# Optimization experiments

Hardware: AMD Instinct MI355X
Metric: run time of the kernel (lower is better)

## Reference

```python
import jax, jax.numpy as jnp
import numpy as np

B, N, D, H, C = 2, 2048, 1024, 16, 3
Dh = D // H


def setup_inputs() -> dict:
    key = jax.random.key(0)
    ks = jax.random.split(key, 6)
    x = jax.random.normal(ks[0], (B, N, D), jnp.float32)
    coords = jax.random.normal(ks[1], (B, N, C), jnp.float32)
    attn_mask = jax.random.normal(ks[2], (N, N), jnp.float32) * 0.1  # additive float bias (2d kind)
    Wqkv = jax.random.normal(ks[3], (D, 3 * D), jnp.float32) / np.sqrt(D)
    bqkv = jax.random.normal(ks[4], (3 * D,), jnp.float32) * 0.01
    rel_weight = jax.random.normal(ks[5], (H, C), jnp.float32) * 0.02
    return {"x": x, "coords": coords, "attn_mask": attn_mask,
            "Wqkv": Wqkv, "bqkv": bqkv, "rel_weight": rel_weight}


def reference(x, coords, attn_mask, Wqkv, bqkv, rel_weight):
    b, n, d = x.shape
    h, dh = rel_weight.shape[0], d // rel_weight.shape[0]
    scale = 1.0 / np.sqrt(float(dh))

    qkv = x @ Wqkv + bqkv                      # [B,N,3D]
    q, k, v = jnp.split(qkv, 3, axis=-1)

    def to_heads(t):
        return t.reshape(b, n, h, dh).transpose(0, 2, 1, 3)  # [B,H,N,Dh]

    qh, kh, vh = to_heads(q), to_heads(k), to_heads(v)

    # scaled dot-product scores (flex_attention applies scale before score_mod)
    scores = jnp.einsum('bhnd,bhmd->bhnm', qh, kh) * scale   # [B,H,N,N]

    # coordinate-derived per-head relative bias: coord_proj[b,h,qi] - coord_proj[b,h,kj]
    coord_proj = jnp.einsum('bnc,hc->bhn', coords.astype(jnp.float32), rel_weight)
    scores = scores + coord_proj[:, :, :, None] - coord_proj[:, :, None, :]

    # additive float mask bias, '2d' kind: shape (N,N) broadcast over B,H
    scores = scores + attn_mask[None, None, :, :]

    attn = jax.nn.softmax(scores, axis=-1)
    out = jnp.einsum('bhnm,bhmd->bhnd', attn, vh)            # [B,H,N,Dh]
    return out.transpose(0, 2, 1, 3).reshape(b, n, d)        # [B,N,D]
```

## Files before the change

### kernel.cpp

```cpp
#include <hip/hip_runtime.h>

typedef _Float16 half8 __attribute__((ext_vector_type(8)));
typedef _Float16 half4 __attribute__((ext_vector_type(4)));
typedef _Float16 half2v __attribute__((ext_vector_type(2)));
typedef float floatx4 __attribute__((ext_vector_type(4)));

#define LOG2E 1.44269504088896f
#define QSCALE 0.18033688011112f

__device__ __forceinline__ void async16(const void* g, void* l) {
    __builtin_amdgcn_global_load_lds(
        (const __attribute__((address_space(1))) unsigned int*)g,
        (__attribute__((address_space(3))) unsigned int*)l, 16, 0, 0);
}
__device__ __forceinline__ half4 pack4(float a, float b, float c, float d) {
    half2v lo = __builtin_bit_cast(half2v, __builtin_amdgcn_cvt_pkrtz(a, b));
    half2v hi = __builtin_bit_cast(half2v, __builtin_amdgcn_cvt_pkrtz(c, d));
    half4 r; r[0] = lo[0]; r[1] = lo[1]; r[2] = hi[0]; r[3] = hi[1];
    return r;
}
__device__ __forceinline__ half8 cat8(half4 lo, half4 hi) {
    half8 r;
    r[0] = lo[0]; r[1] = lo[1]; r[2] = lo[2]; r[3] = lo[3];
    r[4] = hi[0]; r[5] = hi[1]; r[6] = hi[2]; r[7] = hi[3];
    return r;
}

__global__ __launch_bounds__(256) void k_prep(
    const float* __restrict__ x, const float* __restrict__ W,
    const float* __restrict__ coords, const float* __restrict__ rw,
    const float* __restrict__ mask,
    _Float16* __restrict__ xh, _Float16* __restrict__ Wt,
    _Float16* __restrict__ esch, _Float16* __restrict__ maskp) {
    __shared__ float smem[4352];
    int bx = blockIdx.x, tid = threadIdx.x;
    if (bx < 2048) {
        int i = bx * 256 + tid;
        const floatx4* xin = (const floatx4*)x;
        floatx4 a = xin[i * 2];
        floatx4 b = xin[i * 2 + 1];
        half8 h;
        h[0] = (_Float16)a[0]; h[1] = (_Float16)a[1]; h[2] = (_Float16)a[2]; h[3] = (_Float16)a[3];
        h[4] = (_Float16)b[0]; h[5] = (_Float16)b[1]; h[6] = (_Float16)b[2]; h[7] = (_Float16)b[3];
        *(half8*)&xh[i * 8] = h;
    } else if (bx < 5120) {
        int b2 = bx - 2048;
        int n0 = (b2 % 96) * 32, k0 = (b2 / 96) * 32;
        int tx = tid & 31, ty = tid >> 5;
        float (*tile)[33] = (float(*)[33])smem;
        #pragma unroll
        for (int r = 0; r < 4; ++r)
            tile[ty + r * 8][tx] = W[(size_t)(k0 + ty + r * 8) * 3072 + n0 + tx];
        __syncthreads();
        #pragma unroll
        for (int r = 0; r < 4; ++r)
            Wt[(size_t)(n0 + ty + r * 8) * 1024 + k0 + tx] = (_Float16)tile[tx][ty + r * 8];
    } else if (bx < 5376) {
        int idx = (bx - 5120) * 256 + tid;
        int bh = idx >> 11, n = idx & 2047;
        int b = bh >> 4, h = bh & 15;
        const float* c = &coords[(b * 2048 + n) * 3];
        const float* w = &rw[h * 3];
        float v = -LOG2E * (c[0] * w[0] + c[1] * w[1] + c[2] * w[2]);
        esch[idx] = (_Float16)__builtin_amdgcn_exp2f(v);
    } else {
        int bid = bx - 5376;
        int qt = bid >> 5, kt = bid & 31;
        int row0 = qt * 64, col0 = kt * 64;
        int lr = tid >> 2, lc = (tid & 3) * 16;
        #pragma unroll
        for (int j = 0; j < 4; ++j)
            *(floatx4*)&smem[lr * 68 + lc + j * 4] =
                *(const floatx4*)&mask[(size_t)(row0 + lr) * 2048 + col0 + lc + j * 4];
        __syncthreads();
        int w = tid >> 6, lane = tid & 63, quad = lane >> 4, l16 = lane & 15;
        half4* outp = (half4*)maskp + (size_t)((qt * 32 + kt) * 4 + w) * 256 + lane;
        #pragma unroll
        for (int t = 0; t < 4; ++t) {
            floatx4 m = *(const floatx4*)&smem[(w * 16 + l16) * 68 + t * 16 + quad * 4];
            outp[t * 64] = pack4(m[0] * LOG2E, m[1] * LOG2E, m[2] * LOG2E, m[3] * LOG2E);
        }
    }
}

__global__ __launch_bounds__(256) void k_gemm(
    const _Float16* __restrict__ Ah, const _Float16* __restrict__ Bt,
    const float* __restrict__ bias, const _Float16* __restrict__ esch,
    _Float16* __restrict__ qh, _Float16* __restrict__ kh, _Float16* __restrict__ vt) {
    __shared__ _Float16 smem[16384];
    int tid = threadIdx.x;
    int w = tid >> 6, lane = tid & 63;
    int quad = lane >> 4, l16 = lane & 15;
    int m0 = blockIdx.y * 128;
    int n0 = blockIdx.x * 128;
    bool QK = n0 < 2048;
    int mq = (w >> 1) * 64, nq = (w & 1) * 64;
    int c0 = n0 + nq;

    int rl4 = lane >> 2;
    int pb4 = lane & 3;
    floatx4 acc[4][4] = {};

    const _Float16* ap[2];
    const _Float16* bp[2];
    #pragma unroll
    for (int j = 0; j < 2; ++j) {
        int row = w * 32 + j * 16 + rl4;
        int lb = pb4 ^ (row & 3) ^ ((row >> 2) & 3);
        ap[j] = Ah + (size_t)(m0 + row) * 1024 + lb * 8;
        bp[j] = Bt + (size_t)(n0 + row) * 1024 + lb * 8;
    }

    #define GSTAGE(buf) {                                      \
        _Float16* As_ = smem + (buf) * 8192;                   \
        _Float16* Bs_ = As_ + 4096;                            \
        async16(ap[0], &As_[(w * 32) * 32]);                   \
        async16(ap[1], &As_[(w * 32 + 16) * 32]);              \
        async16(bp[0], &Bs_[(w * 32) * 32]);                   \
        async16(bp[1], &Bs_[(w * 32 + 16) * 32]);              \
        ap[0] += 32; ap[1] += 32; bp[0] += 32; bp[1] += 32;    \
    }

    #define GBODY(cur, last) {                                                         \
        __syncthreads();                                                               \
        if (!(last)) GSTAGE((cur) ^ 1);                                                \
        const _Float16* As_ = smem + (cur) * 8192;                                     \
        const _Float16* Bs_ = As_ + 4096;                                              \
        half8 af[4], bf[4];                                                            \
        _Pragma("unroll")                                                              \
        for (int s = 0; s < 4; ++s) {                                                  \
            int ra = mq + s * 16 + l16;                                                \
            af[s] = *(const half8*)&As_[ra * 32 +                                      \
                ((quad ^ (ra & 3) ^ ((ra >> 2) & 3)) << 3)];                           \
            int rb = nq + s * 16 + l16;                                                \
            bf[s] = *(const half8*)&Bs_[rb * 32 +                                      \
                ((quad ^ (rb & 3) ^ ((rb >> 2) & 3)) << 3)];                           \
        }                                                                              \
        if (QK) {                                                                      \
            _Pragma("unroll")                                                          \
            for (int ms = 0; ms < 4; ++ms)                                             \
                _Pragma("unroll")                                                      \
                for (int ns = 0; ns < 4; ++ns)                                         \
                    acc[ms][ns] = __builtin_amdgcn_mfma_f32_16x16x32_f16(              \
                        bf[ns], af[ms], acc[ms][ns], 0, 0, 0);                         \
        } else {                                                                       \
            _Pragma("unroll")                                                          \
            for (int ms = 0; ms < 4; ++ms)                                             \
                _Pragma("unroll")                                                      \
                for (int ns = 0; ns < 4; ++ns)                                         \
                    acc[ms][ns] = __builtin_amdgcn_mfma_f32_16x16x32_f16(              \
                        af[ms], bf[ns], acc[ms][ns], 0, 0, 0);                         \
        }                                                                              \
    }

    GSTAGE(0);
    #pragma unroll 1
    for (int kt2 = 0; kt2 < 15; ++kt2) {
        GBODY(0, false);
        GBODY(1, false);
    }
    GBODY(0, false);
    GBODY(1, true);
    #undef GBODY
    #undef GSTAGE

    __syncthreads();

    _Float16* Ls = smem + w * 2304;
    int rl = lane >> 3, pb = lane & 7;
    int b = (m0 + mq) >> 11, nbase = (m0 + mq) & 2047;
    if (QK) {
        float qsc = (c0 < 1024) ? QSCALE : 1.0f;
        int h2 = c0 >> 6;
        _Float16* dst = (h2 < 16 ? qh : kh) + (size_t)(((b << 4) + (h2 & 15)) * 2048) * 64;
        int d0 = pb << 3;
        #pragma unroll
        for (int p = 0; p < 2; ++p) {
            #pragma unroll
            for (int ns = 0; ns < 4; ++ns) {
                floatx4 b4 = *(const floatx4*)&bias[c0 + ns * 16 + quad * 4];
                #pragma unroll
                for (int m2 = 0; m2 < 2; ++m2) {
                    int ms = p * 2 + m2;
                    floatx4 v;
                    #pragma unroll
                    for (int i = 0; i < 4; ++i) v[i] = (acc[ms][ns][i] + b4[i]) * qsc;
                    *(half4*)&Ls[(m2 * 16 + l16) * 72 + ns * 16 + quad * 4] =
                        pack4(v[0], v[1], v[2], v[3]);
                }
            }
            #pragma unroll
            for (int rep = 0; rep < 4; ++rep) {
                int nl = rep * 8 + rl;
                half8 v = *(const half8*)&Ls[nl * 72 + d0];
                *(half8*)&dst[(size_t)(nbase + p * 32 + nl) * 64 + d0] = v;
            }
        }
    } else {
        int h = (c0 - 2048) >> 6;
        _Float16* dst = vt + (size_t)(((b << 4) + h) * 64) * 2048;
        const _Float16* ePtr = esch + (size_t)((b << 4) + h) * 2048 + nbase + quad * 4;
        float ef[4][4];
        #pragma unroll
        for (int ms = 0; ms < 4; ++ms) {
            half4 e4 = *(const half4*)&ePtr[ms * 16];
            #pragma unroll
            for (int i = 0; i < 4; ++i) ef[ms][i] = (float)e4[i];
        }
        int noff = pb << 3;
        #pragma unroll
        for (int p = 0; p < 2; ++p) {
            #pragma unroll
            for (int n2 = 0; n2 < 2; ++n2) {
                int ns = p * 2 + n2;
                float bv = bias[c0 + ns * 16 + l16];
                #pragma unroll
                for (int ms = 0; ms < 4; ++ms) {
                    *(half4*)&Ls[(n2 * 16 + l16) * 72 + ms * 16 + quad * 4] =
                        pack4((acc[ms][ns][0] + bv) * ef[ms][0],
                              (acc[ms][ns][1] + bv) * ef[ms][1],
                              (acc[ms][ns][2] + bv) * ef[ms][2],
                              (acc[ms][ns][3] + bv) * ef[ms][3]);
                }
            }
            #pragma unroll
            for (int rep = 0; rep < 4; ++rep) {
                int cl = rep * 8 + rl;
                half8 v = *(const half8*)&Ls[cl * 72 + noff];
                *(half8*)&dst[(size_t)(p * 32 + cl) * 2048 + nbase + noff] = v;
            }
        }
    }
}

__global__ __launch_bounds__(256) __attribute__((amdgpu_waves_per_eu(4, 4)))
void k_attn(
    const _Float16* __restrict__ qh, const _Float16* __restrict__ kh,
    const _Float16* __restrict__ vt, const _Float16* __restrict__ maskp,
    const _Float16* __restrict__ esch, float* __restrict__ out) {
    __shared__ _Float16 KV[2][2][4096];
    __shared__ _Float16 es[2048];
    int tid = threadIdx.x;
    int w = tid >> 6, lane = tid & 63;
    int g2 = w >> 1, wq = w & 1;
    int quad = lane >> 4, l16 = lane & 15;
    int bid = blockIdx.x;
    int qt3 = bid & 31, bh = bid >> 5;
    int b = bh >> 4, h = bh & 15;
    int qrow = qt3 * 64 + wq * 32;

    *(half8*)&es[tid * 8] = *(const half8*)&esch[(size_t)bh * 2048 + tid * 8];

    half8 qf[2][2];
    #pragma unroll
    for (int g = 0; g < 2; ++g) {
        const _Float16* qp = &qh[((size_t)bh * 2048 + qrow + g * 16 + l16) * 64];
        qf[g][0] = *(const half8*)&qp[quad * 8];
        qf[g][1] = *(const half8*)&qp[32 + quad * 8];
    }
    floatx4 o0[4] = {}, o1[4] = {};
    floatx4 ol0 = {}, ol1 = {};

    int rl = lane >> 3, pb = lane & 7;
    int swk = (pb ^ rl) << 3;
    const _Float16* kp0 = kh + (size_t)bh * 131072
        + (size_t)(g2 * 1024 + wq * 16 + rl) * 64 + swk;
    const _Float16* kp1 = kp0 + 512;
    int lbs = pb ^ (rl & 7);
    const _Float16* vp0 = vt + (size_t)bh * 131072
        + (size_t)(wq * 32 + 2 * rl + (lbs >> 2)) * 2048 + g2 * 1024 + ((lbs & 3) << 3);
    const _Float16* vp1 = vp0 + 16 * 2048;
    const half4* mp0 = (const half4*)maskp +
        ((size_t)(qt3 * 32 + g2 * 16) * 4 + wq * 2 + 0) * 256 + lane;
    const half4* mp1 = (const half4*)maskp +
        ((size_t)(qt3 * 32 + g2 * 16) * 4 + wq * 2 + 1) * 256 + lane;
    int ecur = g2 * 1024 + quad * 4;

    half4 mC0[2], mC1[2];

    #define STAGE(buf) {                                             \
        async16(kp0, &KV[g2][buf][wq * 1024]);                       \
        async16(kp1, &KV[g2][buf][wq * 1024 + 512]);                 \
        async16(vp0, &KV[g2][buf][2048 + wq * 1024]);                \
        async16(vp1, &KV[g2][buf][2048 + wq * 1024 + 512]);          \
        kp0 += 2048; kp1 += 2048; vp0 += 32; vp1 += 32;              \
    }

    #define MPREF(d) {                                               \
        mC0[0] = mp0[0]; mC0[1] = mp0[64];                           \
        mC1[0] = mp1[0]; mC1[1] = mp1[64];                           \
        mp0 += (d); mp1 += (d);                                      \
    }

    #define BODY(cur, last, md, full) {                                                \
        if (full) {                                                                    \
            __syncthreads();                                                           \
        } else {                                                                       \
            asm volatile("s_waitcnt vmcnt(4)" ::: "memory");                           \
            __builtin_amdgcn_s_barrier();                                              \
        }                                                                              \
        __builtin_amdgcn_sched_barrier(0);            \
        if (!(last)) STAGE((cur) ^ 1);                                                 \
        __builtin_amdgcn_sched_barrier(0);      \
        const _Float16* Ksc = &KV[g2][cur][0];                                         \
        const _Float16* Vsc = &KV[g2][cur][2048];                                      \
        half4 ptl[2][2];                                                               \
        _Pragma("unroll")                                                              \
        for (int t = 0; t < 2; ++t) {                                                  \
            int r = t * 16 + l16;                                                      \
            half8 k0 = *(const half8*)&Ksc[r * 64 + ((quad ^ (r & 7)) << 3)];          \
            half8 k1 = *(const half8*)&Ksc[r * 64 + (((quad + 4) ^ (r & 7)) << 3)];    \
            {                                                                          \
                half4 ml = mC0[t];                                                     \
                floatx4 z;                                                             \
                z[0] = (float)ml[0]; z[1] = (float)ml[1];                              \
                z[2] = (float)ml[2]; z[3] = (float)ml[3];                              \
                z = __builtin_amdgcn_mfma_f32_16x16x32_f16(k0, qf[0][0], z, 0, 0, 0);  \
                z = __builtin_amdgcn_mfma_f32_16x16x32_f16(k1, qf[0][1], z, 0, 0, 0);  \
                ptl[0][t] = pack4(__builtin_amdgcn_exp2f(z[0]),                        \
                                  __builtin_amdgcn_exp2f(z[1]),                        \
                                  __builtin_amdgcn_exp2f(z[2]),                        \
                                  __builtin_amdgcn_exp2f(z[3]));                       \
            }                                                                          \
            {                                                                          \
                half4 ml = mC1[t];                                                     \
                floatx4 z;                                                             \
                z[0] = (float)ml[0]; z[1] = (float)ml[1];                              \
                z[2] = (float)ml[2]; z[3] = (float)ml[3];                              \
                z = __builtin_amdgcn_mfma_f32_16x16x32_f16(k0, qf[1][0], z, 0, 0, 0);  \
                z = __builtin_amdgcn_mfma_f32_16x16x32_f16(k1, qf[1][1], z, 0, 0, 0);  \
                ptl[1][t] = pack4(__builtin_amdgcn_exp2f(z[0]),                        \
                                  __builtin_amdgcn_exp2f(z[1]),                        \
                                  __builtin_amdgcn_exp2f(z[2]),                        \
                                  __builtin_amdgcn_exp2f(z[3]));                       \
            }                                                                          \
        }                                                                              \
        if (!(last)) MPREF(md);                                                        \
        half8 pt8_0 = cat8(ptl[0][0], ptl[0][1]);                                      \
        half8 pt8_1 = cat8(ptl[1][0], ptl[1][1]);                                      \
        {                                                                              \
            half4 e0 = *(const half4*)&es[ecur];                                       \
            half4 e1 = *(const half4*)&es[ecur + 16];                                  \
            half8 ev = cat8(e0, e1);                                                   \
            ol0 = __builtin_amdgcn_mfma_f32_16x16x32_f16(ev, pt8_0, ol0, 0, 0, 0);     \
            ol1 = __builtin_amdgcn_mfma_f32_16x16x32_f16(ev, pt8_1, ol1, 0, 0, 0);     \
        }                                                                              \
        ecur += 32;                                                                    \
        _Pragma("unroll")                                                              \
        for (int dt = 0; dt < 4; ++dt) {                                               \
            int rv = dt * 16 + l16;                                                    \
            int sr = rv >> 1;                                                          \
            int lb0 = ((rv & 1) << 2) | (quad >> 1);                                   \
            half4 vlo = *(const half4*)&Vsc[sr * 64 +                                  \
                ((lb0 ^ (sr & 7)) << 3) + ((quad & 1) << 2)];                          \
            half4 vhi = *(const half4*)&Vsc[sr * 64 +                                  \
                (((lb0 | 2) ^ (sr & 7)) << 3) + ((quad & 1) << 2)];                    \
            half8 vf = cat8(vlo, vhi);                                                 \
            o0[dt] = __builtin_amdgcn_mfma_f32_16x16x32_f16(vf, pt8_0, o0[dt], 0, 0, 0); \
            o1[dt] = __builtin_amdgcn_mfma_f32_16x16x32_f16(vf, pt8_1, o1[dt], 0, 0, 0); \
        }                                                                              \
    }

    STAGE(0);
    MPREF(128);
    BODY(0, false, 896, 1);
    BODY(1, false, 128, 0);
    #pragma unroll 1
    for (int kt2 = 0; kt2 < 14; ++kt2) {
        BODY(0, false, 896, 0);
        BODY(1, false, 128, 0);
    }
    BODY(0, false, 896, 0);
    BODY(1, true, 0, 0);
    #undef BODY
    #undef MPREF
    #undef STAGE

    __syncthreads();
    float* comb = (float*)KV;
    {
        float* dst = comb + ((size_t)w * 17) * 64 + lane;
        if (g2 == 0) {
            #pragma unroll
            for (int dt = 0; dt < 4; ++dt)
                #pragma unroll
                for (int i = 0; i < 4; ++i)
                    dst[(dt * 4 + i) * 64] = o1[dt][i];
            dst[16 * 64] = ol1[0];
        } else {
            #pragma unroll
            for (int dt = 0; dt < 4; ++dt)
                #pragma unroll
                for (int i = 0; i < 4; ++i)
                    dst[(dt * 4 + i) * 64] = o0[dt][i];
            dst[16 * 64] = ol0[0];
        }
    }
    __syncthreads();
    {
        const float* src = comb + ((size_t)(w ^ 2) * 17) * 64 + lane;
        if (g2 == 0) {
            #pragma unroll
            for (int dt = 0; dt < 4; ++dt)
                #pragma unroll
                for (int i = 0; i < 4; ++i)
                    o0[dt][i] += src[(dt * 4 + i) * 64];
            float inv = 1.f / (ol0[0] + src[16 * 64]);
            size_t obase = ((size_t)(b * 2048 + qrow + l16)) * 1024 + h * 64 + quad * 4;
            #pragma unroll
            for (int dt = 0; dt < 4; ++dt) {
                floatx4 r;
                #pragma unroll
                for (int i = 0; i < 4; ++i) r[i] = o0[dt][i] * inv;
                *(floatx4*)&out[obase + dt * 16] = r;
            }
        } else {
            #pragma unroll
            for (int dt = 0; dt < 4; ++dt)
                #pragma unroll
                for (int i = 0; i < 4; ++i)
                    o1[dt][i] += src[(dt * 4 + i) * 64];
            float inv = 1.f / (ol1[0] + src[16 * 64]);
            size_t obase = ((size_t)(b * 2048 + qrow + 16 + l16)) * 1024 + h * 64 + quad * 4;
            #pragma unroll
            for (int dt = 0; dt < 4; ++dt) {
                floatx4 r;
                #pragma unroll
                for (int i = 0; i < 4; ++i) r[i] = o1[dt][i] * inv;
                *(floatx4*)&out[obase + dt * 16] = r;
            }
        }
    }
}

extern "C" void kernel_launch(void* const* d_in, const int* in_sizes, int n_in,
                              void* d_out, int out_size, void* d_ws, size_t ws_size,
                              hipStream_t stream) {
    const float* x      = (const float*)d_in[0];
    const float* coords = (const float*)d_in[1];
    const float* mask   = (const float*)d_in[2];
    const float* Wqkv   = (const float*)d_in[3];
    const float* bqkv   = (const float*)d_in[4];
    const float* rw     = (const float*)d_in[5];
    float* out = (float*)d_out;

    char* ws = (char*)d_ws;
    _Float16* xh    = (_Float16*)(ws);
    _Float16* maskp = (_Float16*)(ws + 8388608);
    _Float16* Wt    = (_Float16*)(ws + 16777216);
    _Float16* qh    = (_Float16*)(ws + 23068672);
    _Float16* kh    = (_Float16*)(ws + 31457280);
    _Float16* vt    = (_Float16*)(ws + 39845888);
    _Float16* esch  = (_Float16*)(ws + 48234496);

    k_prep<<<6400, 256, 0, stream>>>(x, Wqkv, coords, rw, mask, xh, Wt, esch, maskp);
    k_gemm<<<dim3(24, 32), 256, 0, stream>>>(xh, Wt, bqkv, esch, qh, kh, vt);
    k_attn<<<1024, 256, 0, stream>>>(qh, kh, vt, maskp, esch, out);
}
```

Baseline: 187.7 us.

## Load K fragments directly into registers and remap block order for L2 locality

K tiles are no longer staged through LDS. Each lane now prefetches its MFMA K fragments straight from global memory into registers one iteration ahead, next to the mask prefetch. Only V remains in the async LDS double buffer, which halves the shared-memory footprint, and the vmcnt wait is raised to match the extra outstanding loads. The block index is also permuted so that nearby blocks work on different heads or batches, which changes L2 reuse patterns. The tradeoffs are more VGPR pressure, less coalesced K loads, and duplicated K reads across the waves that share a key range.

```diff
diff --git a/kernel.cpp b/kernel.cpp
--- a/kernel.cpp
+++ b/kernel.cpp
@@ -238,14 +238,15 @@
     const _Float16* __restrict__ qh, const _Float16* __restrict__ kh,
     const _Float16* __restrict__ vt, const _Float16* __restrict__ maskp,
     const _Float16* __restrict__ esch, float* __restrict__ out) {
-    __shared__ _Float16 KV[2][2][4096];
-    __shared__ _Float16 es[2048];
+    __shared__ _Float16 shmem[10240];
+    _Float16* es = &shmem[8192];
     int tid = threadIdx.x;
     int w = tid >> 6, lane = tid & 63;
     int g2 = w >> 1, wq = w & 1;
     int quad = lane >> 4, l16 = lane & 15;
     int bid = blockIdx.x;
-    int qt3 = bid & 31, bh = bid >> 5;
+    int lbid = ((bid & 7) << 7) | (bid >> 3);
+    int qt3 = lbid & 31, bh = lbid >> 5;
     int b = bh >> 4, h = bh & 15;
     int qrow = qt3 * 64 + wq * 32;
 
@@ -262,14 +263,12 @@
     floatx4 ol0 = {}, ol1 = {};
 
     int rl = lane >> 3, pb = lane & 7;
-    int swk = (pb ^ rl) << 3;
-    const _Float16* kp0 = kh + (size_t)bh * 131072
-        + (size_t)(g2 * 1024 + wq * 16 + rl) * 64 + swk;
-    const _Float16* kp1 = kp0 + 512;
     int lbs = pb ^ (rl & 7);
     const _Float16* vp0 = vt + (size_t)bh * 131072
         + (size_t)(wq * 32 + 2 * rl + (lbs >> 2)) * 2048 + g2 * 1024 + ((lbs & 3) << 3);
     const _Float16* vp1 = vp0 + 16 * 2048;
+    const _Float16* kgp = kh + (size_t)bh * 131072
+        + (size_t)(g2 * 1024 + l16) * 64 + quad * 8;
     const half4* mp0 = (const half4*)maskp +
         ((size_t)(qt3 * 32 + g2 * 16) * 4 + wq * 2 + 0) * 256 + lane;
     const half4* mp1 = (const half4*)maskp +
@@ -277,13 +276,20 @@
     int ecur = g2 * 1024 + quad * 4;
 
     half4 mC0[2], mC1[2];
+    half8 kA0, kA1, kB0, kB1;
 
     #define STAGE(buf) {                                             \
-        async16(kp0, &KV[g2][buf][wq * 1024]);                       \
-        async16(kp1, &KV[g2][buf][wq * 1024 + 512]);                 \
-        async16(vp0, &KV[g2][buf][2048 + wq * 1024]);                \
-        async16(vp1, &KV[g2][buf][2048 + wq * 1024 + 512]);          \
-        kp0 += 2048; kp1 += 2048; vp0 += 32; vp1 += 32;              \
+        async16(vp0, &shmem[((g2) * 2 + (buf)) * 2048 + wq * 1024]);       \
+        async16(vp1, &shmem[((g2) * 2 + (buf)) * 2048 + wq * 1024 + 512]); \
+        vp0 += 32; vp1 += 32;                                        \
+    }
+
+    #define KPREF() {                                                \
+        kA0 = *(const half8*)kgp;                                    \
+        kA1 = *(const half8*)(kgp + 32);                             \
+        kB0 = *(const half8*)(kgp + 1024);                           \
+        kB1 = *(const half8*)(kgp + 1056);                           \
+        kgp += 2048;                                                 \
     }
 
     #define MPREF(d) {                                               \
@@ -296,46 +302,57 @@
         if (full) {                                                                    \
             __syncthreads();                                                           \
         } else {                                                                       \
-            asm volatile("s_waitcnt vmcnt(4)" ::: "memory");                           \
+            asm volatile("s_waitcnt vmcnt(8)" ::: "memory");                           \
             __builtin_amdgcn_s_barrier();                                              \
         }                                                                              \
         __builtin_amdgcn_sched_barrier(0);            \
         if (!(last)) STAGE((cur) ^ 1);                                                 \
-        __builtin_amdgcn_sched_barrier(0);      \
-        const _Float16* Ksc = &KV[g2][cur][0];                                         \
-        const _Float16* Vsc = &KV[g2][cur][2048];                                      \
+        __builtin_amdgcn_sched_barrier(0);         \
+        const _Float16* Vsc = &shmem[((g2) * 2 + (cur)) * 2048];                       \
         half4 ptl[2][2];                                                               \
-        _Pragma("unroll")                                                              \
-        for (int t = 0; t < 2; ++t) {                                                  \
-            int r = t * 16 + l16;                                                      \
-            half8 k0 = *(const half8*)&Ksc[r * 64 + ((quad ^ (r & 7)) << 3)];          \
-            half8 k1 = *(const half8*)&Ksc[r * 64 + (((quad + 4) ^ (r & 7)) << 3)];    \
-            {                                                                          \
-                half4 ml = mC0[t];                                                     \
-                floatx4 z;                                                             \
-                z[0] = (float)ml[0]; z[1] = (float)ml[1];                              \
-                z[2] = (float)ml[2]; z[3] = (float)ml[3];                              \
-                z = __builtin_amdgcn_mfma_f32_16x16x32_f16(k0, qf[0][0], z, 0, 0, 0);  \
-                z = __builtin_amdgcn_mfma_f32_16x16x32_f16(k1, qf[0][1], z, 0, 0, 0);  \
-                ptl[0][t] = pack4(__builtin_amdgcn_exp2f(z[0]),                        \
-                                  __builtin_amdgcn_exp2f(z[1]),                        \
-                                  __builtin_amdgcn_exp2f(z[2]),                        \
-                                  __builtin_amdgcn_exp2f(z[3]));                       \
-            }                                                                          \
-            {                                                                          \
-                half4 ml = mC1[t];                                                     \
-                floatx4 z;                                                             \
-                z[0] = (float)ml[0]; z[1] = (float)ml[1];                              \
-                z[2] = (float)ml[2]; z[3] = (float)ml[3];                              \
-                z = __builtin_amdgcn_mfma_f32_16x16x32_f16(k0, qf[1][0], z, 0, 0, 0);  \
-                z = __builtin_amdgcn_mfma_f32_16x16x32_f16(k1, qf[1][1], z, 0, 0, 0);  \
-                ptl[1][t] = pack4(__builtin_amdgcn_exp2f(z[0]),                        \
-                                  __builtin_amdgcn_exp2f(z[1]),                        \
-                                  __builtin_amdgcn_exp2f(z[2]),                        \
-                                  __builtin_amdgcn_exp2f(z[3]));                       \
-            }                                                                          \
-        }                                                                              \
-        if (!(last)) MPREF(md);                                                        \
+        {                                                  \
+            half4 ml = mC0[0];                                                         \
+            floatx4 z;                                                                 \
+            z[0] = (float)ml[0]; z[1] = (float)ml[1];                                  \
+            z[2] = (float)ml[2]; z[3] = (float)ml[3];                                  \
+            z = __builtin_amdgcn_mfma_f32_16x16x32_f16(kA0, qf[0][0], z, 0, 0, 0);     \
+            z = __builtin_amdgcn_mfma_f32_16x16x32_f16(kA1, qf[0][1], z, 0, 0, 0);     \
+            ptl[0][0] = pack4(__builtin_amdgcn_exp2f(z[0]),                            \
+                              __builtin_amdgcn_exp2f(z[1]),                            \
+                              __builtin_amdgcn_exp2f(z[2]),                            \
+                              __builtin_amdgcn_exp2f(z[3]));                           \
+            ml = mC1[0];                                                               \
+            z[0] = (float)ml[0]; z[1] = (float)ml[1];                                  \
+            z[2] = (float)ml[2]; z[3] = (float)ml[3];                                  \
+            z = __builtin_amdgcn_mfma_f32_16x16x32_f16(kA0, qf[1][0], z, 0, 0, 0);     \
+            z = __builtin_amdgcn_mfma_f32_16x16x32_f16(kA1, qf[1][1], z, 0, 0, 0);     \
+            ptl[1][0] = pack4(__builtin_amdgcn_exp2f(z[0]),                            \
+                              __builtin_amdgcn_exp2f(z[1]),                            \
+                              __builtin_amdgcn_exp2f(z[2]),                            \
+                              __builtin_amdgcn_exp2f(z[3]));                           \
+        }                                                                              \
+        {                                                  \
+            half4 ml = mC0[1];                                                         \
+            floatx4 z;                                                                 \
+            z[0] = (float)ml[0]; z[1] = (float)ml[1];                                  \
+            z[2] = (float)ml[2]; z[3] = (float)ml[3];                                  \
+            z = __builtin_amdgcn_mfma_f32_16x16x32_f16(kB0, qf[0][0], z, 0, 0, 0);     \
+            z = __builtin_amdgcn_mfma_f32_16x16x32_f16(kB1, qf[0][1], z, 0, 0, 0);     \
+            ptl[0][1] = pack4(__builtin_amdgcn_exp2f(z[0]),                            \
+                              __builtin_amdgcn_exp2f(z[1]),                            \
+                              __builtin_amdgcn_exp2f(z[2]),                            \
+                              __builtin_amdgcn_exp2f(z[3]));                           \
+            ml = mC1[1];                                                               \
+            z[0] = (float)ml[0]; z[1] = (float)ml[1];                                  \
+            z[2] = (float)ml[2]; z[3] = (float)ml[3];                                  \
+            z = __builtin_amdgcn_mfma_f32_16x16x32_f16(kB0, qf[1][0], z, 0, 0, 0);     \
+            z = __builtin_amdgcn_mfma_f32_16x16x32_f16(kB1, qf[1][1], z, 0, 0, 0);     \
+            ptl[1][1] = pack4(__builtin_amdgcn_exp2f(z[0]),                            \
+                              __builtin_amdgcn_exp2f(z[1]),                            \
+                              __builtin_amdgcn_exp2f(z[2]),                            \
+                              __builtin_amdgcn_exp2f(z[3]));                           \
+        }                                                                              \
+        if (!(last)) { KPREF(); MPREF(md); }   \
         half8 pt8_0 = cat8(ptl[0][0], ptl[0][1]);                                      \
         half8 pt8_1 = cat8(ptl[1][0], ptl[1][1]);                                      \
         {                                                                              \
@@ -362,6 +379,7 @@
     }
 
     STAGE(0);
+    KPREF();
     MPREF(128);
     BODY(0, false, 896, 1);
     BODY(1, false, 128, 0);
@@ -374,10 +392,11 @@
     BODY(1, true, 0, 0);
     #undef BODY
     #undef MPREF
+    #undef KPREF
     #undef STAGE
 
     __syncthreads();
-    float* comb = (float*)KV;
+    float* comb = (float*)shmem;
     {
         float* dst = comb + ((size_t)w * 17) * 64 + lane;
         if (g2 == 0) {
```

Result: slower. 222.7 us (+18.6%).
